# Performance work log

Hardware: AMD Instinct MI355X
Metric: run time of the kernel (lower is better)

The kernel has to match this reference:

```python
import jax, jax.numpy as jnp
import numpy as np

B, T, D, L = 16, 4096, 512, 1024

def setup_inputs() -> dict:
    key = jax.random.key(0)
    k1, k2, k3, k4 = jax.random.split(key, 4)
    x = jax.random.normal(k1, (B, T, D), dtype=jnp.float32)
    q = jax.random.normal(k2, (L, D), dtype=jnp.float32)
    fc_w = jax.random.normal(k3, (1, D), dtype=jnp.float32) * (1.0 / np.sqrt(D))
    fc_b = jax.random.normal(k4, (1,), dtype=jnp.float32) * 0.01
    return {"x": x, "q": q, "fc_w": fc_w, "fc_b": fc_b}

def reference(x, q, fc_w, fc_b):
    # att: (B, T, L) label-wise attention scores, softmax over sequence axis T
    att = jnp.einsum('btd,ld->btl', x, q)
    att = jax.nn.softmax(att, axis=1)
    # out: (B, L, D) attention-pooled features per label
    out = jnp.einsum('btl,btd->bld', att, x)
    # linear head to scalar per label -> (B, L)
    return jnp.einsum('bld,od->blo', out, fc_w).squeeze(-1) + fc_b[0]
```

## Files before the change

### kernel.cpp

```cpp
#include <hip/hip_runtime.h>

#define B_ 16
#define T_ 4096
#define D_ 512
#define L_ 1024
#define NTCH (T_ / 64)
#define PPLANE ((size_t)B_ * NTCH * L_)
#define XBLK (B_ * T_ / 16)

typedef _Float16 half8 __attribute__((ext_vector_type(8)));
typedef float float4v __attribute__((ext_vector_type(4)));

__device__ inline void gl_lds(const void* g, void* l) {
    __builtin_amdgcn_global_load_lds(
        (const __attribute__((address_space(1))) unsigned int*)g,
        (__attribute__((address_space(3))) unsigned int*)l, 16, 0, 0);
}

__global__ __launch_bounds__(256) void k_prep(const float* __restrict__ x,
                                              const float* __restrict__ q,
                                              const float* __restrict__ w,
                                              _Float16* __restrict__ xt,
                                              _Float16* __restrict__ qt,
                                              float* __restrict__ y) {
    __shared__ float Xl[16 * 516];
    __shared__ float Yp[64];
    const int tid = threadIdx.x;
    const bool isq = blockIdx.x >= XBLK;
    const int blk = isq ? (blockIdx.x - XBLK) : blockIdx.x;
    const float* bsrc = (isq ? q : x) + (size_t)blk * (16 * 512);
    half8* dst = (half8*)(isq ? qt : xt) + (size_t)blk * 1024;

#pragma unroll
    for (int it = 0; it < 8; ++it) {
        int f = it * 1024 + tid * 4;
        int row = f >> 9, k = f & 511;
        *(float4*)&Xl[row * 516 + k] = *(const float4*)(bsrc + f);
    }
    __syncthreads();

    const int wv = tid >> 6, lane = tid & 63;
    const int row = lane & 15, gq = lane >> 4;
    float acc = 0.f;
#pragma unroll
    for (int it = 0; it < 4; ++it) {
        int kc = it * 4 + wv;
        int k0 = kc * 32 + gq * 8;
        float4 a = *(const float4*)&Xl[row * 516 + k0];
        float4 c = *(const float4*)&Xl[row * 516 + k0 + 4];
        half8 h;
        h[0] = (_Float16)a.x; h[1] = (_Float16)a.y; h[2] = (_Float16)a.z; h[3] = (_Float16)a.w;
        h[4] = (_Float16)c.x; h[5] = (_Float16)c.y; h[6] = (_Float16)c.z; h[7] = (_Float16)c.w;
        dst[kc * 64 + lane] = h;
        if (!isq) {
            float4 wa = *(const float4*)(w + k0);
            float4 wc = *(const float4*)(w + k0 + 4);
            acc = fmaf(a.x, wa.x, acc); acc = fmaf(a.y, wa.y, acc);
            acc = fmaf(a.z, wa.z, acc); acc = fmaf(a.w, wa.w, acc);
            acc = fmaf(c.x, wc.x, acc); acc = fmaf(c.y, wc.y, acc);
            acc = fmaf(c.z, wc.z, acc); acc = fmaf(c.w, wc.w, acc);
        }
    }
    if (!isq) {
        acc += __shfl_xor(acc, 16, 64);
        acc += __shfl_xor(acc, 32, 64);
        if (gq == 0) Yp[wv * 16 + row] = acc;
        __syncthreads();
        if (tid < 16)
            y[blk * 16 + tid] = Yp[tid] + Yp[16 + tid] + Yp[32 + tid] + Yp[48 + tid];
    }
}

__global__ __launch_bounds__(256, 4) void k_mfma(const _Float16* __restrict__ xt,
                                                 const _Float16* __restrict__ qt,
                                                 const float* __restrict__ y,
                                                 float* __restrict__ part) {
    __shared__ half8 S[2048];
    __shared__ float ys[128];

    const int bid  = blockIdx.x;
    const int xcd  = bid & 7;
    const int jj   = bid >> 3;
    const int tile = (xcd << 6) | (jj >> 3);
    const int lblk = jj & 7;
    const int tblk = tile & 31;
    const int b    = tile >> 5;

    const int tid  = threadIdx.x;
    const int lane = tid & 63;
    const int w    = tid >> 6;
    const int tb0  = b * (T_ / 16) + tblk * 8;
    const int lb0  = lblk * 8;

    if (tid < 128) ys[tid] = y[(size_t)b * T_ + tblk * 128 + tid];

    float4v acc[4][4];
#pragma unroll
    for (int i = 0; i < 4; ++i)
#pragma unroll
        for (int j = 0; j < 4; ++j) acc[i][j] = (float4v){0.f, 0.f, 0.f, 0.f};

    const half8* Xg = (const half8*)xt;
    const half8* Qg = (const half8*)qt;
    const int xa = tb0 + 2 * w;
    const int qa = lb0 + 2 * w;
    const int ts = (w >> 1) * 4, ls = (w & 1) * 4;

    for (int kk = 0; kk < D_ / 64; ++kk) {
        const int kc0 = kk * 2;
        __syncthreads();
#pragma unroll
        for (int s = 0; s < 2; ++s) {
            gl_lds(Xg + ((size_t)xa * (D_ / 32) + kc0 + s) * 64 + lane,
                   &S[s * 512 + (2 * w) * 64]);
            gl_lds(Xg + ((size_t)(xa + 1) * (D_ / 32) + kc0 + s) * 64 + lane,
                   &S[s * 512 + (2 * w + 1) * 64]);
            gl_lds(Qg + ((size_t)qa * (D_ / 32) + kc0 + s) * 64 + lane,
                   &S[1024 + s * 512 + (2 * w) * 64]);
            gl_lds(Qg + ((size_t)(qa + 1) * (D_ / 32) + kc0 + s) * 64 + lane,
                   &S[1024 + s * 512 + (2 * w + 1) * 64]);
        }
        __syncthreads();

#pragma unroll
        for (int s = 0; s < 2; ++s) {
            half8 A[4], Bv[4];
#pragma unroll
            for (int i = 0; i < 4; ++i) A[i] = S[s * 512 + (ts + i) * 64 + lane];
#pragma unroll
            for (int j = 0; j < 4; ++j) Bv[j] = S[1024 + s * 512 + (ls + j) * 64 + lane];
#pragma unroll
            for (int i = 0; i < 4; ++i)
#pragma unroll
                for (int j = 0; j < 4; ++j)
                    acc[i][j] = __builtin_amdgcn_mfma_f32_16x16x32_f16(A[i], Bv[j], acc[i][j], 0, 0, 0);
        }
    }

    const int quad = lane >> 4, cl = lane & 15;
    const int tw = (w >> 1) * 64;
    const int tchunk = tblk * 2 + (w >> 1);
    const int lbase = lblk * 128 + (w & 1) * 64;

    float* pm = part;
    float* pz = part + PPLANE;
    float* pn = part + 2 * PPLANE;

#pragma unroll
    for (int j = 0; j < 4; ++j) {
        float m = -1e30f;
#pragma unroll
        for (int i = 0; i < 4; ++i)
#pragma unroll
            for (int r = 0; r < 4; ++r) m = fmaxf(m, acc[i][j][r]);
        float z = 0.f, n = 0.f;
#pragma unroll
        for (int i = 0; i < 4; ++i)
#pragma unroll
            for (int r = 0; r < 4; ++r) {
                float p = __expf(acc[i][j][r] - m);
                z += p;
                n = fmaf(p, ys[tw + i * 16 + quad * 4 + r], n);
            }
#pragma unroll
        for (int msk = 16; msk <= 32; msk <<= 1) {
            float om = __shfl_xor(m, msk, 64);
            float oz = __shfl_xor(z, msk, 64);
            float on = __shfl_xor(n, msk, 64);
            float mn = fmaxf(m, om);
            float s0 = __expf(m - mn), s1 = __expf(om - mn);
            z = fmaf(z, s0, oz * s1);
            n = fmaf(n, s0, on * s1);
            m = mn;
        }
        if (quad == 0) {
            int l = lbase + j * 16 + cl;
            size_t a = ((size_t)b * NTCH + tchunk) * L_ + l;
            pm[a] = m;
            pz[a] = z;
            pn[a] = n;
        }
    }
}

__global__ __launch_bounds__(256) void k_comb_p(const float* __restrict__ part,
                                                const float* __restrict__ fc_b,
                                                float* __restrict__ out) {
    int bl = blockIdx.x * 256 + threadIdx.x;
    int b = bl >> 10, l = bl & (L_ - 1);
    const float* pm = part;
    const float* pz = part + PPLANE;
    const float* pn = part + 2 * PPLANE;
    float m = -1e30f, z = 0.f, n = 0.f;
    for (int c = 0; c < NTCH; ++c) {
        size_t a = ((size_t)b * NTCH + c) * L_ + l;
        float pmv = pm[a], pzv = pz[a], pnv = pn[a];
        float mn = fmaxf(m, pmv);
        float s0 = __expf(m - mn), s1 = __expf(pmv - mn);
        z = fmaf(z, s0, pzv * s1);
        n = fmaf(n, s0, pnv * s1);
        m = mn;
    }
    out[bl] = n / z + fc_b[0];
}

#define NC 8
#define TC (T_ / NC)
#define BT 128
#define BL 128
#define KK 32

__global__ __launch_bounds__(256) void k_y(const float* __restrict__ x,
                                           const float* __restrict__ w,
                                           float* __restrict__ y) {
    int row  = (blockIdx.x * 256 + threadIdx.x) >> 6;
    int lane = threadIdx.x & 63;
    const float* r = x + (size_t)row * D_;
    float s = 0.f;
#pragma unroll
    for (int k = 0; k < D_; k += 64) s = fmaf(r[k + lane], w[k + lane], s);
#pragma unroll
    for (int o = 32; o > 0; o >>= 1) s += __shfl_xor(s, o, 64);
    if (lane == 0) y[row] = s;
}

__global__ __launch_bounds__(256, 2) void k_main(const float* __restrict__ x,
                                                 const float* __restrict__ q,
                                                 const float* __restrict__ y,
                                                 float* __restrict__ part) {
    __shared__ float Xs[KK][BT + 4];
    __shared__ float Qs[KK][BL + 4];
    const int tid = threadIdx.x;
    const int ty = tid & 15, tx = tid >> 4;
    const int lb = blockIdx.x * BL, chunk = blockIdx.y, b = blockIdx.z;
    const int g = tid & 7, r0 = tid >> 3;

    float run_m[8], run_z[8], run_n[8];
#pragma unroll
    for (int j = 0; j < 8; ++j) { run_m[j] = -1e30f; run_z[j] = 0.f; run_n[j] = 0.f; }

    for (int tt = 0; tt < TC; tt += BT) {
        const int t0 = chunk * TC + tt;
        float s[8][8];
#pragma unroll
        for (int i = 0; i < 8; ++i)
#pragma unroll
            for (int j = 0; j < 8; ++j) s[i][j] = 0.f;
        for (int kc = 0; kc < D_; kc += KK) {
            __syncthreads();
#pragma unroll
            for (int p = 0; p < 4; ++p) {
                int rr = p * 32 + r0;
                float4 vx = *(const float4*)(x + ((size_t)b * T_ + t0 + rr) * D_ + kc + g * 4);
                float4 vq = *(const float4*)(q + (size_t)(lb + rr) * D_ + kc + g * 4);
                Xs[g * 4 + 0][rr] = vx.x; Xs[g * 4 + 1][rr] = vx.y;
                Xs[g * 4 + 2][rr] = vx.z; Xs[g * 4 + 3][rr] = vx.w;
                Qs[g * 4 + 0][rr] = vq.x; Qs[g * 4 + 1][rr] = vq.y;
                Qs[g * 4 + 2][rr] = vq.z; Qs[g * 4 + 3][rr] = vq.w;
            }
            __syncthreads();
#pragma unroll
            for (int k = 0; k < KK; ++k) {
                float4 a0 = *(const float4*)&Xs[k][ty * 4];
                float4 a1 = *(const float4*)&Xs[k][64 + ty * 4];
                float4 b0 = *(const float4*)&Qs[k][tx * 4];
                float4 b1 = *(const float4*)&Qs[k][64 + tx * 4];
                float av[8] = {a0.x, a0.y, a0.z, a0.w, a1.x, a1.y, a1.z, a1.w};
                float bv[8] = {b0.x, b0.y, b0.z, b0.w, b1.x, b1.y, b1.z, b1.w};
#pragma unroll
                for (int i = 0; i < 8; ++i)
#pragma unroll
                    for (int j = 0; j < 8; ++j) s[i][j] = fmaf(av[i], bv[j], s[i][j]);
            }
        }
        float yv[8];
#pragma unroll
        for (int i = 0; i < 8; ++i) {
            int tl = (i < 4) ? (ty * 4 + i) : (64 + ty * 4 + (i - 4));
            yv[i] = y[(size_t)b * T_ + t0 + tl];
        }
#pragma unroll
        for (int j = 0; j < 8; ++j) {
            float mt = s[0][j];
#pragma unroll
            for (int i = 1; i < 8; ++i) mt = fmaxf(mt, s[i][j]);
            float mn = fmaxf(run_m[j], mt);
            float sc = __expf(run_m[j] - mn);
            float z = run_z[j] * sc, n = run_n[j] * sc;
#pragma unroll
            for (int i = 0; i < 8; ++i) {
                float p = __expf(s[i][j] - mn);
                z += p;
                n = fmaf(p, yv[i], n);
            }
            run_m[j] = mn; run_z[j] = z; run_n[j] = n;
        }
    }
#pragma unroll
    for (int msk = 1; msk < 16; msk <<= 1) {
#pragma unroll
        for (int j = 0; j < 8; ++j) {
            float om = __shfl_xor(run_m[j], msk, 64);
            float oz = __shfl_xor(run_z[j], msk, 64);
            float on = __shfl_xor(run_n[j], msk, 64);
            float mn = fmaxf(run_m[j], om);
            float s0 = __expf(run_m[j] - mn), s1 = __expf(om - mn);
            run_z[j] = fmaf(run_z[j], s0, oz * s1);
            run_n[j] = fmaf(run_n[j], s0, on * s1);
            run_m[j] = mn;
        }
    }
    if (ty == 0) {
#pragma unroll
        for (int j = 0; j < 8; ++j) {
            int ll = (j < 4) ? (tx * 4 + j) : (64 + tx * 4 + (j - 4));
            size_t idx = ((size_t)(b * L_ + lb + ll) * NC + chunk) * 3;
            part[idx + 0] = run_m[j];
            part[idx + 1] = run_z[j];
            part[idx + 2] = run_n[j];
        }
    }
}

__global__ __launch_bounds__(256) void k_comb_f(const float* __restrict__ part,
                                                const float* __restrict__ fc_b,
                                                float* __restrict__ out) {
    int bl = blockIdx.x * 256 + threadIdx.x;
    float m = -1e30f, z = 0.f, n = 0.f;
    for (int c = 0; c < NC; ++c) {
        size_t idx = ((size_t)bl * NC + c) * 3;
        float pm = part[idx + 0], pz = part[idx + 1], pn = part[idx + 2];
        float mn = fmaxf(m, pm);
        float s0 = __expf(m - mn), s1 = __expf(pm - mn);
        z = fmaf(z, s0, pz * s1);
        n = fmaf(n, s0, pn * s1);
        m = mn;
    }
    out[bl] = n / z + fc_b[0];
}

extern "C" void kernel_launch(void* const* d_in, const int* in_sizes, int n_in,
                              void* d_out, int out_size, void* d_ws, size_t ws_size,
                              hipStream_t stream) {
    const float* x    = (const float*)d_in[0];
    const float* q    = (const float*)d_in[1];
    const float* fc_w = (const float*)d_in[2];
    const float* fc_b = (const float*)d_in[3];
    float* out = (float*)d_out;
    float* ws  = (float*)d_ws;

    const size_t Y_F    = (size_t)B_ * T_;
    const size_t PART_F = 3 * PPLANE;
    const size_t XT_H   = (size_t)B_ * T_ * D_;
    const size_t QT_H   = (size_t)L_ * D_;
    const size_t need   = (Y_F + PART_F) * 4 + (XT_H + QT_H) * 2;

    if (ws_size >= need) {
        float* y    = ws;
        float* part = ws + Y_F;
        _Float16* xt = (_Float16*)(ws + Y_F + PART_F);
        _Float16* qt = xt + XT_H;
        k_prep<<<XBLK + L_ / 16, 256, 0, stream>>>(x, q, fc_w, xt, qt, y);
        k_mfma<<<4096, 256, 0, stream>>>(xt, qt, y, part);
        k_comb_p<<<B_ * L_ / 256, 256, 0, stream>>>(part, fc_b, out);
    } else {
        float* y    = ws;
        float* part = ws + Y_F;
        k_y   <<<B_ * T_ / 4, 256, 0, stream>>>(x, fc_w, y);
        k_main<<<dim3(L_ / BL, NC, B_), 256, 0, stream>>>(x, q, y, part);
        k_comb_f<<<B_ * L_ / 256, 256, 0, stream>>>(part, fc_b, out);
    }
}
```

Baseline: 282.0 us.

## Enlarge MFMA tile to 256x128 per block and swizzle prep LDS layout

The MFMA score kernel now computes a 256(T) x 128(L) tile per block with an 8x4 fragment grid per wave instead of 128x128. Each Q fragment loaded into LDS is therefore reused across twice as many T rows, and the grid shrinks to 2048 blocks. Partial softmax chunks cover 128 T rows, so NTCH drops to 32 and the combine kernel reads half as much partial data. The bigger accumulator set raises register pressure, so launch bounds drop to 2 blocks per SM. Separately, the prep kernel replaces row padding in LDS with an XOR swizzle to avoid bank conflicts.

```diff
diff --git a/kernel.cpp b/kernel.cpp
--- a/kernel.cpp
+++ b/kernel.cpp
@@ -4,7 +4,7 @@
 #define T_ 4096
 #define D_ 512
 #define L_ 1024
-#define NTCH (T_ / 64)
+#define NTCH 32
 #define PPLANE ((size_t)B_ * NTCH * L_)
 #define XBLK (B_ * T_ / 16)
 
@@ -23,7 +23,7 @@
                                               _Float16* __restrict__ xt,
                                               _Float16* __restrict__ qt,
                                               float* __restrict__ y) {
-    __shared__ float Xl[16 * 516];
+    __shared__ float Xl[16 * 512];
     __shared__ float Yp[64];
     const int tid = threadIdx.x;
     const bool isq = blockIdx.x >= XBLK;
@@ -35,7 +35,8 @@
     for (int it = 0; it < 8; ++it) {
         int f = it * 1024 + tid * 4;
         int row = f >> 9, k = f & 511;
-        *(float4*)&Xl[row * 516 + k] = *(const float4*)(bsrc + f);
+        int pc = (k >> 2) ^ (row & 7);
+        *(float4*)&Xl[row * 512 + pc * 4] = *(const float4*)(bsrc + f);
     }
     __syncthreads();
 
@@ -45,9 +46,10 @@
 #pragma unroll
     for (int it = 0; it < 4; ++it) {
         int kc = it * 4 + wv;
+        int c0 = kc * 8 + gq * 2;
         int k0 = kc * 32 + gq * 8;
-        float4 a = *(const float4*)&Xl[row * 516 + k0];
-        float4 c = *(const float4*)&Xl[row * 516 + k0 + 4];
+        float4 a = *(const float4*)&Xl[row * 512 + ((c0 ^ (row & 7)) << 2)];
+        float4 c = *(const float4*)&Xl[row * 512 + (((c0 + 1) ^ (row & 7)) << 2)];
         half8 h;
         h[0] = (_Float16)a.x; h[1] = (_Float16)a.y; h[2] = (_Float16)a.z; h[3] = (_Float16)a.w;
         h[4] = (_Float16)c.x; h[5] = (_Float16)c.y; h[6] = (_Float16)c.z; h[7] = (_Float16)c.w;
@@ -71,66 +73,68 @@
     }
 }
 
-__global__ __launch_bounds__(256, 4) void k_mfma(const _Float16* __restrict__ xt,
+__global__ __launch_bounds__(256, 2) void k_mfma(const _Float16* __restrict__ xt,
                                                  const _Float16* __restrict__ qt,
                                                  const float* __restrict__ y,
                                                  float* __restrict__ part) {
-    __shared__ half8 S[2048];
-    __shared__ float ys[128];
+    __shared__ half8 S[3072];
+    __shared__ float ys[256];
 
     const int bid  = blockIdx.x;
     const int xcd  = bid & 7;
     const int jj   = bid >> 3;
-    const int tile = (xcd << 6) | (jj >> 3);
+    const int tile = (xcd << 5) | (jj >> 3);
     const int lblk = jj & 7;
-    const int tblk = tile & 31;
-    const int b    = tile >> 5;
+    const int tblk = tile & 15;
+    const int b    = tile >> 4;
 
     const int tid  = threadIdx.x;
     const int lane = tid & 63;
     const int w    = tid >> 6;
-    const int tb0  = b * (T_ / 16) + tblk * 8;
+    const int wt   = w >> 1, wl = w & 1;
+    const int tb0  = b * (T_ / 16) + tblk * 16;
     const int lb0  = lblk * 8;
 
-    if (tid < 128) ys[tid] = y[(size_t)b * T_ + tblk * 128 + tid];
-
-    float4v acc[4][4];
-#pragma unroll
-    for (int i = 0; i < 4; ++i)
+    ys[tid] = y[(size_t)b * T_ + tblk * 256 + tid];
+
+    float4v acc[8][4];
+#pragma unroll
+    for (int i = 0; i < 8; ++i)
 #pragma unroll
         for (int j = 0; j < 4; ++j) acc[i][j] = (float4v){0.f, 0.f, 0.f, 0.f};
 
     const half8* Xg = (const half8*)xt;
     const half8* Qg = (const half8*)qt;
-    const int xa = tb0 + 2 * w;
-    const int qa = lb0 + 2 * w;
-    const int ts = (w >> 1) * 4, ls = (w & 1) * 4;
 
     for (int kk = 0; kk < D_ / 64; ++kk) {
-        const int kc0 = kk * 2;
         __syncthreads();
 #pragma unroll
         for (int s = 0; s < 2; ++s) {
-            gl_lds(Xg + ((size_t)xa * (D_ / 32) + kc0 + s) * 64 + lane,
-                   &S[s * 512 + (2 * w) * 64]);
-            gl_lds(Xg + ((size_t)(xa + 1) * (D_ / 32) + kc0 + s) * 64 + lane,
-                   &S[s * 512 + (2 * w + 1) * 64]);
-            gl_lds(Qg + ((size_t)qa * (D_ / 32) + kc0 + s) * 64 + lane,
-                   &S[1024 + s * 512 + (2 * w) * 64]);
-            gl_lds(Qg + ((size_t)(qa + 1) * (D_ / 32) + kc0 + s) * 64 + lane,
-                   &S[1024 + s * 512 + (2 * w + 1) * 64]);
+            const int kc = kk * 2 + s;
+#pragma unroll
+            for (int p = 0; p < 4; ++p) {
+                int xb = p * 4 + w;
+                gl_lds(Xg + ((size_t)(tb0 + xb) * (D_ / 32) + kc) * 64 + lane,
+                       &S[s * 1536 + xb * 64]);
+            }
+#pragma unroll
+            for (int p = 0; p < 2; ++p) {
+                int qb = p * 4 + w;
+                gl_lds(Qg + ((size_t)(lb0 + qb) * (D_ / 32) + kc) * 64 + lane,
+                       &S[s * 1536 + 1024 + qb * 64]);
+            }
         }
         __syncthreads();
 
 #pragma unroll
         for (int s = 0; s < 2; ++s) {
-            half8 A[4], Bv[4];
-#pragma unroll
-            for (int i = 0; i < 4; ++i) A[i] = S[s * 512 + (ts + i) * 64 + lane];
-#pragma unroll
-            for (int j = 0; j < 4; ++j) Bv[j] = S[1024 + s * 512 + (ls + j) * 64 + lane];
-#pragma unroll
-            for (int i = 0; i < 4; ++i)
+            half8 A[8], Bv[4];
+#pragma unroll
+            for (int i = 0; i < 8; ++i) A[i] = S[s * 1536 + (wt * 8 + i) * 64 + lane];
+#pragma unroll
+            for (int j = 0; j < 4; ++j) Bv[j] = S[s * 1536 + 1024 + (wl * 4 + j) * 64 + lane];
+#pragma unroll
+            for (int i = 0; i < 8; ++i)
 #pragma unroll
                 for (int j = 0; j < 4; ++j)
                     acc[i][j] = __builtin_amdgcn_mfma_f32_16x16x32_f16(A[i], Bv[j], acc[i][j], 0, 0, 0);
@@ -138,9 +142,8 @@
     }
 
     const int quad = lane >> 4, cl = lane & 15;
-    const int tw = (w >> 1) * 64;
-    const int tchunk = tblk * 2 + (w >> 1);
-    const int lbase = lblk * 128 + (w & 1) * 64;
+    const int tchunk = tblk * 2 + wt;
+    const int lbase  = lblk * 128 + wl * 64;
 
     float* pm = part;
     float* pz = part + PPLANE;
@@ -150,17 +153,17 @@
     for (int j = 0; j < 4; ++j) {
         float m = -1e30f;
 #pragma unroll
-        for (int i = 0; i < 4; ++i)
+        for (int i = 0; i < 8; ++i)
 #pragma unroll
             for (int r = 0; r < 4; ++r) m = fmaxf(m, acc[i][j][r]);
         float z = 0.f, n = 0.f;
 #pragma unroll
-        for (int i = 0; i < 4; ++i)
+        for (int i = 0; i < 8; ++i)
 #pragma unroll
             for (int r = 0; r < 4; ++r) {
                 float p = __expf(acc[i][j][r] - m);
                 z += p;
-                n = fmaf(p, ys[tw + i * 16 + quad * 4 + r], n);
+                n = fmaf(p, ys[wt * 128 + i * 16 + quad * 4 + r], n);
             }
 #pragma unroll
         for (int msk = 16; msk <= 32; msk <<= 1) {
@@ -351,6 +354,7 @@
 
     const size_t Y_F    = (size_t)B_ * T_;
     const size_t PART_F = 3 * PPLANE;
+    const size_t PARTF_FALLBACK = (size_t)B_ * L_ * NC * 3;
     const size_t XT_H   = (size_t)B_ * T_ * D_;
     const size_t QT_H   = (size_t)L_ * D_;
     const size_t need   = (Y_F + PART_F) * 4 + (XT_H + QT_H) * 2;
@@ -361,11 +365,12 @@
         _Float16* xt = (_Float16*)(ws + Y_F + PART_F);
         _Float16* qt = xt + XT_H;
         k_prep<<<XBLK + L_ / 16, 256, 0, stream>>>(x, q, fc_w, xt, qt, y);
-        k_mfma<<<4096, 256, 0, stream>>>(xt, qt, y, part);
+        k_mfma<<<2048, 256, 0, stream>>>(xt, qt, y, part);
         k_comb_p<<<B_ * L_ / 256, 256, 0, stream>>>(part, fc_b, out);
     } else {
         float* y    = ws;
         float* part = ws + Y_F;
+        (void)PARTF_FALLBACK;
         k_y   <<<B_ * T_ / 4, 256, 0, stream>>>(x, fc_w, y);
         k_main<<<dim3(L_ / BL, NC, B_), 256, 0, stream>>>(x, q, y, part);
         k_comb_f<<<B_ * L_ / 256, 256, 0, stream>>>(part, fc_b, out);
```

Result: no change. 277.4 us (-1.6%).
